# Optimization experiments

Hardware: AMD Instinct MI355X
Metric: run time of the kernel (lower is better)

The kernel has to match this reference:

```python
import jax, jax.numpy as jnp
import numpy as np

N, D, H, E, K = 4096, 1024, 2048, 8, 2


def setup_inputs() -> dict:
    key = jax.random.key(0)
    ks = jax.random.split(key, 4)
    x = jax.random.normal(ks[0], (N, D), dtype=jnp.float32)
    w_gate = jax.random.normal(ks[1], (D, E), dtype=jnp.float32) * 0.02
    w1 = jax.random.normal(ks[2], (E, D, H), dtype=jnp.float32) * (1.0 / np.sqrt(D))
    b1 = jnp.zeros((E, H), dtype=jnp.float32)
    w2 = jax.random.normal(ks[3], (E, H, D), dtype=jnp.float32) * (1.0 / np.sqrt(H))
    b2 = jnp.zeros((E, D), dtype=jnp.float32)
    return {"x": x, "w_gate": w_gate, "w1": w1, "b1": b1, "w2": w2, "b2": b2}


def reference(x, w_gate, w1, b1, w2, b2):
    # --- top-k gating ---
    logits = x @ w_gate                      # [N, E]
    top_vals, top_idx = jax.lax.top_k(logits, K)   # [N, K]
    gates_k = jax.nn.softmax(top_vals, axis=-1)    # softmax over selected experts
    # scatter sparse gates into dense [N, E] combine weights (zeros off top-k)
    gates = jnp.zeros((x.shape[0], E), dtype=x.dtype)
    gates = gates.at[jnp.arange(x.shape[0])[:, None], top_idx].set(gates_k)
    # --- expert FFNs (computed densely over experts, combined sparsely) ---
    h = jax.nn.gelu(jnp.einsum('nd,edh->neh', x, w1) + b1[None])   # [N, E, H]
    y = jnp.einsum('neh,ehd->ned', h, w2) + b2[None]               # [N, E, D]
    out = jnp.einsum('ne,ned->nd', gates, y)                        # [N, D]
    return out
```

## Files before the change

### kernel.cpp

```cpp
#include <hip/hip_runtime.h>
#include <math.h>
#include <stdint.h>

#define N_TOK 4096
#define DIM   1024
#define HID   2048
#define NE    8
#define NROWS (N_TOK * 2)
#define LDST  72
#define OBST  144
#define MAXSLOT 72
#define TPT   16

typedef __attribute__((ext_vector_type(8))) short bf16x8;
typedef __attribute__((ext_vector_type(4))) float f32x4;

__device__ __forceinline__ unsigned short f2bf(float f) {
    union { unsigned int i; float f; } v; v.f = f;
    unsigned int u = v.i;
    return (unsigned short)((u + 0x7FFFu + ((u >> 16) & 1u)) >> 16);
}
__device__ __forceinline__ int clampi(int v, int lo, int hi) {
    return v < lo ? lo : (v > hi ? hi : v);
}
__device__ __forceinline__ void cvt8(const float* p, unsigned short* o) {
    float4 a = *(const float4*)p;
    float4 b = *(const float4*)(p + 4);
    o[0] = f2bf(a.x); o[1] = f2bf(a.y); o[2] = f2bf(a.z); o[3] = f2bf(a.w);
    o[4] = f2bf(b.x); o[5] = f2bf(b.y); o[6] = f2bf(b.z); o[7] = f2bf(b.w);
}
__device__ __forceinline__ float fast_gelu(float v) {
    float c = 0.7978845608028654f * (v + 0.044715f * v * v * v);
    float t = 1.f - 2.f / (1.f + __expf(2.f * c));
    return 0.5f * v * (1.f + t);
}
__device__ __forceinline__ void gload_lds16(const void* g, void* l) {
    __builtin_amdgcn_global_load_lds(
        (const __attribute__((address_space(1))) unsigned int*)g,
        (__attribute__((address_space(3))) unsigned int*)l,
        16, 0, 0);
}

__global__ __launch_bounds__(256) void gate_kernel(
    const float* __restrict__ x, const float* __restrict__ wg,
    unsigned short* __restrict__ top_e, float* __restrict__ top_g)
{
    int wave = threadIdx.x >> 6;
    int lane = threadIdx.x & 63;
    int n = blockIdx.x * 4 + wave;
    if (n >= N_TOK) return;
    float acc[NE];
#pragma unroll
    for (int e = 0; e < NE; e++) acc[e] = 0.f;
    const float* xrow = x + (size_t)n * DIM;
    for (int d = lane; d < DIM; d += 64) {
        float xv = xrow[d];
        float4 wa = *(const float4*)(wg + (size_t)d * NE);
        float4 wb = *(const float4*)(wg + (size_t)d * NE + 4);
        acc[0] += xv * wa.x; acc[1] += xv * wa.y;
        acc[2] += xv * wa.z; acc[3] += xv * wa.w;
        acc[4] += xv * wb.x; acc[5] += xv * wb.y;
        acc[6] += xv * wb.z; acc[7] += xv * wb.w;
    }
#pragma unroll
    for (int e = 0; e < NE; e++) {
        float v = acc[e];
#pragma unroll
        for (int off = 32; off > 0; off >>= 1) v += __shfl_xor(v, off, 64);
        acc[e] = v;
    }
    if (lane == 0) {
        int e0 = 0; float v0 = acc[0];
#pragma unroll
        for (int e = 1; e < NE; e++) if (acc[e] > v0) { v0 = acc[e]; e0 = e; }
        int e1 = (e0 == 0) ? 1 : 0; float v1 = acc[e1];
#pragma unroll
        for (int e = 0; e < NE; e++) if (e != e0 && acc[e] > v1) { v1 = acc[e]; e1 = e; }
        float s = expf(v1 - v0);
        float g0 = 1.f / (1.f + s);
        float g1 = s / (1.f + s);
        top_e[n] = (unsigned short)(e0 | (e1 << 8));
        top_g[2 * n + 0] = g0;
        top_g[2 * n + 1] = g1;
    }
}

__global__ __launch_bounds__(256) void scatter_plan_kernel(
    const unsigned short* __restrict__ top_e, const float* __restrict__ top_g,
    int* __restrict__ row_tok, float* __restrict__ row_gate, int* __restrict__ map)
{
    __shared__ int lpre[256][NE];
    __shared__ int etot[NE];
    __shared__ int ebase[NE];
    int t = threadIdx.x;

    unsigned long long c64 = 0ull;
    unsigned short te[TPT];
#pragma unroll
    for (int i = 0; i < TPT; i++) {
        int v = top_e[t * TPT + i];
        te[i] = (unsigned short)v;
        c64 += 1ull << ((v & 7) * 8);
        c64 += 1ull << (((v >> 8) & 7) * 8);
    }
#pragma unroll
    for (int e = 0; e < NE; e++) lpre[t][e] = (int)((c64 >> (e * 8)) & 0xFF);
    __syncthreads();

    if (t < NE) {
        int s = 0;
        for (int i = 0; i < 256; i++) { int c = lpre[i][t]; lpre[i][t] = s; s += c; }
        etot[t] = s;
    }
    __syncthreads();
    if (t == 0) {
        int b = 0;
#pragma unroll
        for (int e = 0; e < NE; e++) { ebase[e] = b; b += etot[e]; }
        int s = 0; b = 0;
        for (int e = 0; e < NE; e++) {
            int c = clampi(etot[e], 0, NROWS);
            for (int mb = 0; mb * 128 < c && s < MAXSLOT; mb++) {
                int nv = c - mb * 128; if (nv > 128) nv = 128;
                map[s++] = ((b + mb * 128) << 18) | (nv << 10) | e;
            }
            b += c;
        }
        for (; s < MAXSLOT; s++) map[s] = -1;
    }
    __syncthreads();

#pragma unroll
    for (int i = 0; i < TPT; i++) {
        int n = t * TPT + i;
        int v = te[i];
#pragma unroll
        for (int k = 0; k < 2; k++) {
            int e = (k ? (v >> 8) : v) & 7;
            int r = clampi(ebase[e] + lpre[t][e]++, 0, NROWS - 1);
            row_tok[r]  = (n << 1) | k;
            row_gate[r] = top_g[2 * n + k];
        }
    }
}

__global__ __launch_bounds__(256) void pack_x_kernel(
    const float* __restrict__ x, unsigned short* __restrict__ xb)
{
    size_t i = (size_t)(blockIdx.x * 256 + threadIdx.x) * 8;
    unsigned short o[8];
    cvt8(x + i, o);
    *(uint4*)(xb + i) = *(uint4*)o;
}

__global__ __launch_bounds__(256) void transpose_kernel(
    const float* __restrict__ in, unsigned short* __restrict__ outp, int K, int N)
{
    int e  = blockIdx.z;
    int kb = blockIdx.x;
    int nb = blockIdx.y;
    __shared__ __align__(16) unsigned short tile[64 * LDST];
    int t = threadIdx.x;

    int r = t >> 2, cq = t & 3;
    const float* sp = in + ((size_t)e * K + kb * 64 + r) * N + nb * 64 + cq * 16;
    unsigned short v[16];
    cvt8(sp, v);
    cvt8(sp + 8, v + 8);
    *(uint4*)(&tile[r * LDST + cq * 16 + 0]) = *(uint4*)(v + 0);
    *(uint4*)(&tile[r * LDST + cq * 16 + 8]) = *(uint4*)(v + 8);
    __syncthreads();

    int c = t >> 2, kq = t & 3;
    unsigned short o[16];
#pragma unroll
    for (int i = 0; i < 16; i++) o[i] = tile[(kq * 16 + i) * LDST + c];
    unsigned short* dp = outp + ((size_t)e * N + nb * 64 + c) * K + kb * 64 + kq * 16;
    *(uint4*)(dp + 0) = *(uint4*)(o + 0);
    *(uint4*)(dp + 8) = *(uint4*)(o + 8);
}

__global__ __launch_bounds__(256) void ffn1_fast4(
    const unsigned short* __restrict__ xb,
    const unsigned short* __restrict__ w1t,
    const float* __restrict__ b1,
    const int* __restrict__ map,
    const int* __restrict__ row_tok,
    unsigned short* __restrict__ h)
{
    int lid = blockIdx.x;
    int logical = (lid & 7) * (MAXSLOT * 16 / 8) + (lid >> 3);
    int nb   = logical & 15;
    int slot = logical >> 4;

    int mv = map[slot];
    if (mv < 0) return;
    int e      = mv & 0x3FF;
    int nvalid = (mv >> 10) & 0xFF;
    int gr0    = ((unsigned)mv) >> 18;

    __shared__ __align__(16) unsigned short lds[4 * 8192];
    __shared__ int ltok[128];

    int t = threadIdx.x;
    if (t < 128) {
        int rl = clampi(t, 0, nvalid - 1);
        int idx = clampi(gr0 + rl, 0, NROWS - 1);
        ltok[t] = clampi(row_tok[idx] >> 1, 0, N_TOK - 1);
    }
    __syncthreads();

    const int n0 = nb * 128;
    int w = t >> 6;
    const unsigned short* ga[4];
    const unsigned short* gb[4];
    int lofs[4];
#pragma unroll
    for (int i = 0; i < 4; i++) {
        int idx = i * 256 + t;
        int row = idx >> 3, cc = idx & 7;
        int ccs = cc ^ (row & 7);
        ga[i] = xb + (size_t)ltok[row] * DIM + ccs * 8;
        gb[i] = w1t + ((size_t)e * HID + n0 + row) * DIM + ccs * 8;
        lofs[i] = i * 2048 + w * 512;
    }

    int lane = t & 63, quad = lane >> 4, ln = lane & 15;
    int wr = w >> 1, wc = w & 1;
    int xr = ln & 7;
    f32x4 acc[4][4];
#pragma unroll
    for (int i = 0; i < 4; i++)
#pragma unroll
        for (int j = 0; j < 4; j++) acc[i][j] = (f32x4){0.f, 0.f, 0.f, 0.f};

#pragma unroll
    for (int i = 0; i < 4; i++) {
        gload_lds16(ga[i], lds + lofs[i]);
        gload_lds16(gb[i], lds + 8192 + lofs[i]);
    }
    __syncthreads();

    int cur = 0;
    for (int kt = 0; kt < DIM / 64; kt++) {
        int nxt = cur ^ 1;
        if (kt + 1 < DIM / 64) {
            int k0 = (kt + 1) * 64;
            unsigned short* dA = lds + nxt * 16384;
            unsigned short* dB = dA + 8192;
#pragma unroll
            for (int i = 0; i < 4; i++) {
                gload_lds16(ga[i] + k0, dA + lofs[i]);
                gload_lds16(gb[i] + k0, dB + lofs[i]);
            }
        }
        const unsigned short* sA = lds + cur * 16384;
        const unsigned short* sB = sA + 8192;
#pragma unroll
        for (int kk = 0; kk < 2; kk++) {
            bf16x8 af[4], bf[4];
#pragma unroll
            for (int s = 0; s < 4; s++)
                af[s] = *(const bf16x8*)(&sA[(wr * 64 + s * 16 + ln) * 64 + (((kk * 4 + quad) ^ xr) * 8)]);
#pragma unroll
            for (int s = 0; s < 4; s++)
                bf[s] = *(const bf16x8*)(&sB[(wc * 64 + s * 16 + ln) * 64 + (((kk * 4 + quad) ^ xr) * 8)]);
#pragma unroll
            for (int i = 0; i < 4; i++)
#pragma unroll
                for (int j = 0; j < 4; j++)
                    acc[i][j] = __builtin_amdgcn_mfma_f32_16x16x32_bf16(af[i], bf[j], acc[i][j], 0, 0, 0);
        }
        __syncthreads();
        cur = nxt;
    }

    unsigned short* ob = lds;
#pragma unroll
    for (int j = 0; j < 4; j++) {
        int colL = wc * 64 + j * 16 + ln;
        float bias = b1[e * HID + n0 + colL];
#pragma unroll
        for (int i = 0; i < 4; i++) {
#pragma unroll
            for (int r = 0; r < 4; r++) {
                int m = wr * 64 + i * 16 + quad * 4 + r;
                ob[m * OBST + colL] = f2bf(fast_gelu(acc[i][j][r] + bias));
            }
        }
    }
    __syncthreads();
#pragma unroll
    for (int it = 0; it < 8; it++) {
        int idx = it * 256 + t;
        int m = idx >> 4, ch = idx & 15;
        if (m < nvalid)
            *(uint4*)(h + (size_t)(gr0 + m) * HID + n0 + ch * 8) = *(const uint4*)(ob + m * OBST + ch * 8);
    }
}

__global__ __launch_bounds__(256) void ffn2_fast6(
    const unsigned short* __restrict__ h,
    const unsigned short* __restrict__ w2t,
    const float* __restrict__ b2,
    const int* __restrict__ map,
    const int* __restrict__ row_tok,
    const float* __restrict__ row_gate,
    float* __restrict__ out,
    float* __restrict__ ybuf1)
{
    int lid = blockIdx.x;
    int logical = (lid & 7) * (MAXSLOT * 8 / 8) + (lid >> 3);
    int nb   = logical & 7;
    int slot = logical >> 3;

    int mv = map[slot];
    if (mv < 0) return;
    int e      = mv & 0x3FF;
    int nvalid = (mv >> 10) & 0xFF;
    int gr0    = ((unsigned)mv) >> 18;

    __shared__ __align__(16) unsigned short lds[4 * 8192];
    __shared__ int   ltok2[128];
    __shared__ float lgate[128];

    int t = threadIdx.x;
    if (t < 128) {
        int rl = clampi(t, 0, nvalid - 1);
        int idx = clampi(gr0 + rl, 0, NROWS - 1);
        ltok2[t] = clampi(row_tok[idx], 0, 2 * N_TOK - 1);
        lgate[t] = row_gate[idx];
    }
    __syncthreads();

    const int n0 = nb * 128;
    int w = t >> 6;
    const unsigned short* ga[4];
    const unsigned short* gb[4];
    int lofs[4];
#pragma unroll
    for (int i = 0; i < 4; i++) {
        int idx = i * 256 + t;
        int row = idx >> 3, cc = idx & 7;
        int ccs = cc ^ (row & 7);
        int arow = clampi(gr0 + row, 0, NROWS - 1);
        ga[i] = h + (size_t)arow * HID + ccs * 8;
        gb[i] = w2t + ((size_t)e * DIM + n0 + row) * HID + ccs * 8;
        lofs[i] = i * 2048 + w * 512;
    }

    int lane = t & 63, quad = lane >> 4, ln = lane & 15;
    int wr = w >> 1, wc = w & 1;
    int xr = ln & 7;
    f32x4 acc[4][4];
#pragma unroll
    for (int i = 0; i < 4; i++)
#pragma unroll
        for (int j = 0; j < 4; j++) acc[i][j] = (f32x4){0.f, 0.f, 0.f, 0.f};

#pragma unroll
    for (int i = 0; i < 4; i++) {
        gload_lds16(ga[i], lds + lofs[i]);
        gload_lds16(gb[i], lds + 8192 + lofs[i]);
    }
    __syncthreads();

    int cur = 0;
    for (int kt = 0; kt < HID / 64; kt++) {
        int nxt = cur ^ 1;
        if (kt + 1 < HID / 64) {
            int k0 = (kt + 1) * 64;
            unsigned short* dA = lds + nxt * 16384;
            unsigned short* dB = dA + 8192;
#pragma unroll
            for (int i = 0; i < 4; i++) {
                gload_lds16(ga[i] + k0, dA + lofs[i]);
                gload_lds16(gb[i] + k0, dB + lofs[i]);
            }
        }
        const unsigned short* sA = lds + cur * 16384;
        const unsigned short* sB = sA + 8192;
#pragma unroll
        for (int kk = 0; kk < 2; kk++) {
            bf16x8 af[4], bf[4];
#pragma unroll
            for (int s = 0; s < 4; s++)
                af[s] = *(const bf16x8*)(&sA[(wr * 64 + s * 16 + ln) * 64 + (((kk * 4 + quad) ^ xr) * 8)]);
#pragma unroll
            for (int s = 0; s < 4; s++)
                bf[s] = *(const bf16x8*)(&sB[(wc * 64 + s * 16 + ln) * 64 + (((kk * 4 + quad) ^ xr) * 8)]);
#pragma unroll
            for (int i = 0; i < 4; i++)
#pragma unroll
                for (int j = 0; j < 4; j++)
                    acc[i][j] = __builtin_amdgcn_mfma_f32_16x16x32_bf16(af[i], bf[j], acc[i][j], 0, 0, 0);
        }
        __syncthreads();
        cur = nxt;
    }

#pragma unroll
    for (int j = 0; j < 4; j++) {
        int col = n0 + wc * 64 + j * 16 + ln;
        float bias = b2[e * DIM + col];
#pragma unroll
        for (int i = 0; i < 4; i++) {
#pragma unroll
            for (int r = 0; r < 4; r++) {
                int m = wr * 64 + i * 16 + quad * 4 + r;
                if (m < nvalid) {
                    int rt  = ltok2[m];
                    int tok = rt >> 1;
                    float vv = (acc[i][j][r] + bias) * lgate[m];
                    float* dst = (rt & 1) ? ybuf1 : out;
                    dst[(size_t)tok * DIM + col] = vv;
                }
            }
        }
    }
}

__global__ __launch_bounds__(256) void combine_kernel(
    float4* __restrict__ out4, const float4* __restrict__ y4)
{
    int i = blockIdx.x * 256 + threadIdx.x;
    float4 a = out4[i];
    float4 b = y4[i];
    out4[i] = make_float4(a.x + b.x, a.y + b.y, a.z + b.z, a.w + b.w);
}

__global__ __launch_bounds__(256) void zero_out_kernel(float* __restrict__ out) {
    int i = blockIdx.x * 256 + threadIdx.x;
    out[i] = 0.f;
}

extern "C" void kernel_launch(void* const* d_in, const int* in_sizes, int n_in,
                              void* d_out, int out_size, void* d_ws, size_t ws_size,
                              hipStream_t stream) {
    const float* x  = (const float*)d_in[0];
    const float* wg = (const float*)d_in[1];
    const float* w1 = (const float*)d_in[2];
    const float* b1 = (const float*)d_in[3];
    const float* w2 = (const float*)d_in[4];
    const float* b2 = (const float*)d_in[5];
    float* out = (float*)d_out;

    char* ws = (char*)d_ws;
    unsigned short* top_e    = (unsigned short*)(ws + 256);
    float*          top_g    = (float*)(ws + 8448);
    int*            row_tok  = (int*)(ws + 41216);
    float*          row_gate = (float*)(ws + 73984);
    int*            map      = (int*)(ws + 106752);

    const size_t WT_OFF    = (size_t)1 << 17;
    const size_t HBUF_OFF  = WT_OFF + (size_t)NE * DIM * HID * 2;
    const size_t YBUF_OFF  = HBUF_OFF + (size_t)NROWS * HID * 2;
    const size_t NEEDED    = YBUF_OFF + (size_t)N_TOK * DIM * 4;

    if (ws_size < NEEDED) {
        zero_out_kernel<<<dim3(N_TOK * DIM / 256), dim3(256), 0, stream>>>(out);
        return;
    }

    unsigned short* wt    = (unsigned short*)(ws + WT_OFF);
    unsigned short* hbuf  = (unsigned short*)(ws + HBUF_OFF);
    float*          ybuf1 = (float*)(ws + YBUF_OFF);
    unsigned short* xb    = (unsigned short*)(ws + YBUF_OFF);

    gate_kernel<<<dim3(N_TOK / 4), dim3(256), 0, stream>>>(x, wg, top_e, top_g);
    scatter_plan_kernel<<<dim3(1), dim3(256), 0, stream>>>(top_e, top_g, row_tok, row_gate, map);
    pack_x_kernel<<<dim3(N_TOK * DIM / (256 * 8)), dim3(256), 0, stream>>>(x, xb);
    transpose_kernel<<<dim3(DIM / 64, HID / 64, NE), dim3(256), 0, stream>>>(w1, wt, DIM, HID);
    ffn1_fast4<<<dim3(MAXSLOT * 16), dim3(256), 0, stream>>>(xb, wt, b1, map, row_tok, hbuf);
    transpose_kernel<<<dim3(HID / 64, DIM / 64, NE), dim3(256), 0, stream>>>(w2, wt, HID, DIM);
    ffn2_fast6<<<dim3(MAXSLOT * 8), dim3(256), 0, stream>>>(hbuf, wt, b2, map, row_tok, row_gate, out, ybuf1);
    combine_kernel<<<dim3(N_TOK * DIM / 1024), dim3(256), 0, stream>>>((float4*)out, (const float4*)ybuf1);
}
```

Before: 373.4 us.

## Schedule FFN tiles per XCD by expert with overflow work lists

The scatter planner now emits explicit per-XCD work lists for both FFN kernels rather than a flat slot map. Each of the 8 XCD lanes (blockIdx mod 8) gets a fixed-capacity queue filled first with tiles of one expert, so that expert's weights stay in that XCD's L2. Tiles beyond a queue's capacity spill into the remaining queue slots. This adds serial work in the single-thread planner and a fixed grid padded with early-exit blocks.

```diff
diff --git a/kernel.cpp b/kernel.cpp
--- a/kernel.cpp
+++ b/kernel.cpp
@@ -11,6 +11,8 @@
 #define OBST  144
 #define MAXSLOT 72
 #define TPT   16
+#define CAP1  144
+#define CAP2  72
 
 typedef __attribute__((ext_vector_type(8))) short bf16x8;
 typedef __attribute__((ext_vector_type(4))) float f32x4;
@@ -87,11 +89,13 @@
 
 __global__ __launch_bounds__(256) void scatter_plan_kernel(
     const unsigned short* __restrict__ top_e, const float* __restrict__ top_g,
-    int* __restrict__ row_tok, float* __restrict__ row_gate, int* __restrict__ map)
+    int* __restrict__ row_tok, float* __restrict__ row_gate,
+    int* __restrict__ work1, int* __restrict__ work2)
 {
     __shared__ int lpre[256][NE];
     __shared__ int etot[NE];
     __shared__ int ebase[NE];
+    __shared__ int ovf[MAXSLOT * 16];
     int t = threadIdx.x;
 
     unsigned long long c64 = 0ull;
@@ -117,16 +121,46 @@
         int b = 0;
 #pragma unroll
         for (int e = 0; e < NE; e++) { ebase[e] = b; b += etot[e]; }
-        int s = 0; b = 0;
+        int slotG[MAXSLOT], slotV[MAXSLOT], slotE[MAXSLOT];
+        int S = 0; b = 0;
         for (int e = 0; e < NE; e++) {
             int c = clampi(etot[e], 0, NROWS);
-            for (int mb = 0; mb * 128 < c && s < MAXSLOT; mb++) {
+            for (int mb = 0; mb * 128 < c && S < MAXSLOT; mb++) {
                 int nv = c - mb * 128; if (nv > 128) nv = 128;
-                map[s++] = ((b + mb * 128) << 18) | (nv << 10) | e;
+                slotG[S] = b + mb * 128; slotV[S] = nv; slotE[S] = e; S++;
             }
             b += c;
         }
-        for (; s < MAXSLOT; s++) map[s] = -1;
+        {
+            int cap[NE], wp[NE]; int no = 0;
+            for (int x = 0; x < NE; x++) { cap[x] = CAP1; wp[x] = x * CAP1; }
+            for (int s = 0; s < S; s++) {
+                int e = slotE[s];
+                for (int j = 0; j < 16; j++) {
+                    int item = (slotG[s] << 16) | (slotV[s] << 8) | (e << 4) | j;
+                    if (cap[e] > 0) { work1[wp[e]++] = item; cap[e]--; }
+                    else ovf[no++] = item;
+                }
+            }
+            int oi = 0;
+            for (int x = 0; x < NE; x++)
+                while (cap[x] > 0) { work1[wp[x]++] = (oi < no) ? ovf[oi++] : -1; cap[x]--; }
+        }
+        {
+            int cap[NE], wp[NE]; int no = 0;
+            for (int x = 0; x < NE; x++) { cap[x] = CAP2; wp[x] = x * CAP2; }
+            for (int s = 0; s < S; s++) {
+                int e = slotE[s];
+                for (int j = 0; j < 8; j++) {
+                    int item = (slotG[s] << 16) | (slotV[s] << 8) | (e << 4) | j;
+                    if (cap[e] > 0) { work2[wp[e]++] = item; cap[e]--; }
+                    else ovf[no++] = item;
+                }
+            }
+            int oi = 0;
+            for (int x = 0; x < NE; x++)
+                while (cap[x] > 0) { work2[wp[x]++] = (oi < no) ? ovf[oi++] : -1; cap[x]--; }
+        }
     }
     __syncthreads();
 
@@ -180,24 +214,21 @@
     *(uint4*)(dp + 8) = *(uint4*)(o + 8);
 }
 
-__global__ __launch_bounds__(256) void ffn1_fast4(
+__global__ __launch_bounds__(256) void ffn1_fast5(
     const unsigned short* __restrict__ xb,
     const unsigned short* __restrict__ w1t,
     const float* __restrict__ b1,
-    const int* __restrict__ map,
+    const int* __restrict__ work1,
     const int* __restrict__ row_tok,
     unsigned short* __restrict__ h)
 {
     int lid = blockIdx.x;
-    int logical = (lid & 7) * (MAXSLOT * 16 / 8) + (lid >> 3);
-    int nb   = logical & 15;
-    int slot = logical >> 4;
-
-    int mv = map[slot];
-    if (mv < 0) return;
-    int e      = mv & 0x3FF;
-    int nvalid = (mv >> 10) & 0xFF;
-    int gr0    = ((unsigned)mv) >> 18;
+    int wv = work1[(lid & 7) * CAP1 + (lid >> 3)];
+    if (wv < 0) return;
+    int nb     = wv & 15;
+    int e      = (wv >> 4) & 7;
+    int nvalid = (wv >> 8) & 0xFF;
+    int gr0    = ((unsigned)wv) >> 16;
 
     __shared__ __align__(16) unsigned short lds[4 * 8192];
     __shared__ int ltok[128];
@@ -299,26 +330,23 @@
     }
 }
 
-__global__ __launch_bounds__(256) void ffn2_fast6(
+__global__ __launch_bounds__(256) void ffn2_fast7(
     const unsigned short* __restrict__ h,
     const unsigned short* __restrict__ w2t,
     const float* __restrict__ b2,
-    const int* __restrict__ map,
+    const int* __restrict__ work2,
     const int* __restrict__ row_tok,
     const float* __restrict__ row_gate,
     float* __restrict__ out,
     float* __restrict__ ybuf1)
 {
     int lid = blockIdx.x;
-    int logical = (lid & 7) * (MAXSLOT * 8 / 8) + (lid >> 3);
-    int nb   = logical & 7;
-    int slot = logical >> 3;
-
-    int mv = map[slot];
-    if (mv < 0) return;
-    int e      = mv & 0x3FF;
-    int nvalid = (mv >> 10) & 0xFF;
-    int gr0    = ((unsigned)mv) >> 18;
+    int wv = work2[(lid & 7) * CAP2 + (lid >> 3)];
+    if (wv < 0) return;
+    int nb     = wv & 15;
+    int e      = (wv >> 4) & 7;
+    int nvalid = (wv >> 8) & 0xFF;
+    int gr0    = ((unsigned)wv) >> 16;
 
     __shared__ __align__(16) unsigned short lds[4 * 8192];
     __shared__ int   ltok2[128];
@@ -450,7 +478,8 @@
     float*          top_g    = (float*)(ws + 8448);
     int*            row_tok  = (int*)(ws + 41216);
     float*          row_gate = (float*)(ws + 73984);
-    int*            map      = (int*)(ws + 106752);
+    int*            work1    = (int*)(ws + 106752);
+    int*            work2    = (int*)(ws + 111360);
 
     const size_t WT_OFF    = (size_t)1 << 17;
     const size_t HBUF_OFF  = WT_OFF + (size_t)NE * DIM * HID * 2;
@@ -468,11 +497,11 @@
     unsigned short* xb    = (unsigned short*)(ws + YBUF_OFF);
 
     gate_kernel<<<dim3(N_TOK / 4), dim3(256), 0, stream>>>(x, wg, top_e, top_g);
-    scatter_plan_kernel<<<dim3(1), dim3(256), 0, stream>>>(top_e, top_g, row_tok, row_gate, map);
+    scatter_plan_kernel<<<dim3(1), dim3(256), 0, stream>>>(top_e, top_g, row_tok, row_gate, work1, work2);
     pack_x_kernel<<<dim3(N_TOK * DIM / (256 * 8)), dim3(256), 0, stream>>>(x, xb);
     transpose_kernel<<<dim3(DIM / 64, HID / 64, NE), dim3(256), 0, stream>>>(w1, wt, DIM, HID);
-    ffn1_fast4<<<dim3(MAXSLOT * 16), dim3(256), 0, stream>>>(xb, wt, b1, map, row_tok, hbuf);
+    ffn1_fast5<<<dim3(NE * CAP1), dim3(256), 0, stream>>>(xb, wt, b1, work1, row_tok, hbuf);
     transpose_kernel<<<dim3(HID / 64, DIM / 64, NE), dim3(256), 0, stream>>>(w2, wt, HID, DIM);
-    ffn2_fast6<<<dim3(MAXSLOT * 8), dim3(256), 0, stream>>>(hbuf, wt, b2, map, row_tok, row_gate, out, ybuf1);
+    ffn2_fast7<<<dim3(NE * CAP2), dim3(256), 0, stream>>>(hbuf, wt, b2, work2, row_tok, row_gate, out, ybuf1);
     combine_kernel<<<dim3(N_TOK * DIM / 1024), dim3(256), 0, stream>>>((float4*)out, (const float4*)ybuf1);
 }
```

After: 606.4 us. +62.4%, slower.
